# Kernel optimization log

Hardware: AMD Instinct MI355X
Metric: run time of the kernel (lower is better)

## Reference

```python
import jax, jax.numpy as jnp
import numpy as np

EPS = 1e-5


def hyper_graph_conv(x, elements, W, b):
    """x: [B, C, N] vertex features; elements: [M, 8] vertex ids per hex element.
    Gather 8 vertex features per element, apply Linear(8C -> 8Co) on the
    concatenated features, then scatter-mean the 8 outputs back to vertices.
    Returns [B, Co, N]."""
    B, C, N = x.shape
    M = elements.shape[0]
    Co = W.shape[0] // 8
    g = x[:, :, elements]                      # [B, C, M, 8]
    g = jnp.transpose(g, (0, 2, 3, 1)).reshape(B, M, 8 * C)   # [B, M, 8C]
    h = jnp.einsum('bmk,ok->bmo', g, W) + b    # [B, M, 8Co]
    h = h.reshape(B, M * 8, Co)                # per-(element,corner) vertex outputs
    flat = elements.reshape(-1)                # [M*8]
    out = jnp.zeros((B, N, Co), dtype=x.dtype).at[:, flat, :].add(h)
    cnt = jnp.zeros((N,), dtype=x.dtype).at[flat].add(1.0)
    out = out / jnp.maximum(cnt, 1.0)[None, :, None]
    return jnp.transpose(out, (0, 2, 1))       # [B, Co, N]


def batch_norm(x, gamma, beta):
    # BatchNorm1d in training mode over [B, C, N]: stats over (B, N)
    mean = jnp.mean(x, axis=(0, 2), keepdims=True)
    var = jnp.mean(jnp.square(x - mean), axis=(0, 2), keepdims=True)
    xn = (x - mean) * jax.lax.rsqrt(var + EPS)
    return xn * gamma[None, :, None] + beta[None, :, None]


def setup_inputs() -> dict:
    key = jax.random.key(0)
    ks = jax.random.split(key, 8)
    B, Cin, Cout, N, M = 4, 8, 16, 100000, 98304
    return {
        'x': jax.random.normal(ks[0], (B, Cin, N), dtype=jnp.float32),
        'elements': jax.random.randint(ks[1], (M, 8), 0, N, dtype=jnp.int32),
        'W1': jax.random.normal(ks[2], (8 * Cout, 8 * Cin), dtype=jnp.float32) * (1.0 / np.sqrt(8 * Cin)),
        'b1': jnp.zeros((8 * Cout,), dtype=jnp.float32),
        'gamma1': jnp.ones((Cout,), dtype=jnp.float32),
        'beta1': jnp.zeros((Cout,), dtype=jnp.float32),
        'W2': jax.random.normal(ks[3], (8 * Cout, 8 * Cout), dtype=jnp.float32) * (1.0 / np.sqrt(8 * Cout)),
        'b2': jnp.zeros((8 * Cout,), dtype=jnp.float32),
        'gamma2': jnp.ones((Cout,), dtype=jnp.float32),
        'beta2': jnp.zeros((Cout,), dtype=jnp.float32),
        'Wskip': jax.random.normal(ks[4], (Cout, Cin), dtype=jnp.float32) * (1.0 / np.sqrt(Cin)),
        'bskip': jnp.zeros((Cout,), dtype=jnp.float32),
    }


def reference(x, elements, W1, b1, gamma1, beta1, W2, b2, gamma2, beta2, Wskip, bskip):
    out = hyper_graph_conv(x, elements, W1, b1)        # [B, Cout, N]
    out = jax.nn.relu(batch_norm(out, gamma1, beta1))
    out = hyper_graph_conv(out, elements, W2, b2)      # [B, Cout, N]
    out = batch_norm(out, gamma2, beta2)
    skip = jnp.einsum('bcn,oc->bon', x, Wskip) + bskip[None, :, None]  # Conv1d k=1
    out = jax.nn.relu(out + skip)
    return out
```

## Files before the change

kernel.cpp:

```cpp
#include <hip/hip_runtime.h>

#define NB 4
#define CIN 8
#define CO 16
#define NV 100000
#define NM 98304
#define NPOS (NM*8)
#define NBLK ((NV+255)/256)
#define RED_NWV 8192

typedef short s16x8 __attribute__((ext_vector_type(8)));
typedef float f32x4 __attribute__((ext_vector_type(4)));
typedef unsigned short u16;
typedef unsigned int u32;

#define OFF_CNT   0
#define OFF_NEXT  400128
#define OFF_STAT  800256
#define OFF_ROWS  800640
#define OFF_BSUM  1200768
#define OFF_POS   1202432
#define OFF_XTB   4348160
#define OFF_W1B   10748160
#define OFF_W2B   10764544
#define OFF_H1    10797312
#define OFF_ACC   23597312
#define OFF_HBUF  49197312
#define WS_NEED   149860608

static __device__ __forceinline__ u16 f2bf(float f){
  union { float f; u32 u; } v; v.f = f;
  u32 r = v.u + 0x7fffu + ((v.u >> 16) & 1u);
  return (u16)(r >> 16);
}
static __device__ __forceinline__ float bf2f_lo(u32 w){
  union { u32 u; float f; } v; v.u = w << 16; return v.f;
}
static __device__ __forceinline__ float bf2f_hi(u32 w){
  union { u32 u; float f; } v; v.u = w & 0xffff0000u; return v.f;
}
static __device__ __forceinline__ u32 pk2(float a, float b){
  return (u32)f2bf(a) | (((u32)f2bf(b)) << 16);
}

__global__ __launch_bounds__(256) void k_hist(const int* __restrict__ elem,
    const float* __restrict__ W1, const float* __restrict__ W2,
    int* __restrict__ cnt, u16* __restrict__ w1b, u16* __restrict__ w2b)
{
  const int T1 = NPOS;
  const int T2 = T1 + 128*64;
  const int T3 = T2 + 128*128;
  int stride = gridDim.x*blockDim.x;
  for (int i = blockIdx.x*blockDim.x + threadIdx.x; i < T3; i += stride){
    if (i < T1) { atomicAdd(cnt + elem[i], 1); }
    else if (i < T2){ int j = i - T1; w1b[j] = f2bf(W1[j]); }
    else { int j = i - T2; w2b[j] = f2bf(W2[j]); }
  }
}

__global__ __launch_bounds__(256) void k_xt(const float* __restrict__ x, u16* __restrict__ xtb)
{
  __shared__ float tile[32][257];
  int t = threadIdx.x;
  int v0 = blockIdx.x*256;
  #pragma unroll
  for (int r = 0; r < 32; r++){
    int v = v0 + t;
    tile[r][t] = (v < NV) ? x[(size_t)r*NV + v] : 0.f;
  }
  __syncthreads();
  int v = v0 + t;
  if (v < NV){
    u16 o[32] __attribute__((aligned(16)));
    #pragma unroll
    for (int r = 0; r < 32; r++) o[r] = f2bf(tile[r][t]);
    uint4* dst = (uint4*)(xtb + (size_t)v*32);
    #pragma unroll
    for (int k = 0; k < 4; k++) dst[k] = *(uint4*)(o + k*8);
  }
}

__global__ __launch_bounds__(256) void k_scan_a(const int* __restrict__ cnt, int* __restrict__ bsum)
{
  int v = blockIdx.x*256 + threadIdx.x;
  int x = (v < NV) ? cnt[v] : 0;
  #pragma unroll
  for (int off = 32; off > 0; off >>= 1) x += __shfl_down(x, off);
  __shared__ int ls[4];
  int wid = threadIdx.x >> 6, lane = threadIdx.x & 63;
  if (lane == 0) ls[wid] = x;
  __syncthreads();
  if (threadIdx.x == 0) bsum[blockIdx.x] = ls[0] + ls[1] + ls[2] + ls[3];
}

__global__ void k_scan_b(int* __restrict__ bsum)
{
  int lane = threadIdx.x & 63;
  int base = 0;
  for (int i0 = 0; i0 < NBLK; i0 += 64){
    int i = i0 + lane;
    int xv = (i < NBLK) ? bsum[i] : 0;
    int incl = xv;
    #pragma unroll
    for (int off = 1; off <= 32; off <<= 1){
      int y = __shfl_up(incl, off);
      if (lane >= off) incl += y;
    }
    if (i < NBLK) bsum[i] = base + incl - xv;
    base += __shfl(incl, 63);
  }
}

__global__ __launch_bounds__(256) void k_scan_c(const int* __restrict__ cnt,
    const int* __restrict__ bsum, int* __restrict__ rows)
{
  int v = blockIdx.x*256 + threadIdx.x;
  int x = (v < NV) ? cnt[v] : 0;
  int incl = x;
  #pragma unroll
  for (int off = 1; off <= 32; off <<= 1){
    int y = __shfl_up(incl, off);
    if ((threadIdx.x & 63) >= off) incl += y;
  }
  __shared__ int wt[4];
  int wid = threadIdx.x >> 6, lane = threadIdx.x & 63;
  if (lane == 63) wt[wid] = incl;
  __syncthreads();
  int woff = 0;
  for (int w = 0; w < 4; w++) if (w < wid) woff += wt[w];
  if (v < NV) rows[v] = bsum[blockIdx.x] + woff + incl - x;
}

__global__ __launch_bounds__(256) void k_pos(const int* __restrict__ elem,
    const int* __restrict__ rows, int* __restrict__ next, int* __restrict__ pos)
{
  int i = blockIdx.x*256 + threadIdx.x;
  if (i < NPOS){
    int v = elem[i];
    int old = atomicAdd(next + v, 1);
    pos[i] = rows[v] + old;
  }
}

__global__ __launch_bounds__(256) void k_conv1(const int* __restrict__ elem,
    const u16* __restrict__ xtb, const u16* __restrict__ w1b,
    const float* __restrict__ b1, const int* __restrict__ pos, u16* __restrict__ hbuf)
{
  const int lane = threadIdx.x & 63;
  const int col = lane & 15, kg = lane >> 4, b = lane & 3;
  s16x8 wf[8][2];
  #pragma unroll
  for (int j2 = 0; j2 < 8; j2++)
    #pragma unroll
    for (int t = 0; t < 2; t++)
      wf[j2][t] = *(const s16x8*)(w1b + (j2*16 + col)*64 + t*32 + kg*8);
  float bb[8];
  #pragma unroll
  for (int j2 = 0; j2 < 8; j2++) bb[j2] = b1[j2*16 + col];

  int wave = (int)((blockIdx.x*blockDim.x + threadIdx.x) >> 6);
  int g0 = wave, g1 = wave + 12288;
  int ma0 = g0*4 + (col >> 2), ma1 = g1*4 + (col >> 2);
  int me0 = g0*4 + kg,         me1 = g1*4 + kg;

  int e00 = elem[ma0*8 + kg], e01 = elem[ma0*8 + 4 + kg];
  int e10 = elem[ma1*8 + kg], e11 = elem[ma1*8 + 4 + kg];
  int4 p0l = *(const int4*)(pos + me0*8), p0h = *(const int4*)(pos + me0*8 + 4);
  int4 p1l = *(const int4*)(pos + me1*8), p1h = *(const int4*)(pos + me1*8 + 4);
  s16x8 a00 = *(const s16x8*)(xtb + (size_t)e00*32 + b*8);
  s16x8 a01 = *(const s16x8*)(xtb + (size_t)e01*32 + b*8);
  s16x8 a10 = *(const s16x8*)(xtb + (size_t)e10*32 + b*8);
  s16x8 a11 = *(const s16x8*)(xtb + (size_t)e11*32 + b*8);

  int pe0[8] = {p0l.x,p0l.y,p0l.z,p0l.w,p0h.x,p0h.y,p0h.z,p0h.w};
  int pe1[8] = {p1l.x,p1l.y,p1l.z,p1l.w,p1h.x,p1h.y,p1h.z,p1h.w};

  #pragma unroll
  for (int j2 = 0; j2 < 8; j2++){
    f32x4 c = {0.f,0.f,0.f,0.f};
    c = __builtin_amdgcn_mfma_f32_16x16x32_bf16(a00, wf[j2][0], c, 0, 0, 0);
    c = __builtin_amdgcn_mfma_f32_16x16x32_bf16(a01, wf[j2][1], c, 0, 0, 0);
    uint2 d; d.x = pk2(c[0]+bb[j2], c[1]+bb[j2]); d.y = pk2(c[2]+bb[j2], c[3]+bb[j2]);
    *(uint2*)(hbuf + (size_t)pe0[j2]*64 + col*4) = d;
  }
  #pragma unroll
  for (int j2 = 0; j2 < 8; j2++){
    f32x4 c = {0.f,0.f,0.f,0.f};
    c = __builtin_amdgcn_mfma_f32_16x16x32_bf16(a10, wf[j2][0], c, 0, 0, 0);
    c = __builtin_amdgcn_mfma_f32_16x16x32_bf16(a11, wf[j2][1], c, 0, 0, 0);
    uint2 d; d.x = pk2(c[0]+bb[j2], c[1]+bb[j2]); d.y = pk2(c[2]+bb[j2], c[3]+bb[j2]);
    *(uint2*)(hbuf + (size_t)pe1[j2]*64 + col*4) = d;
  }
}

__global__ __launch_bounds__(256) void k_conv2(const int* __restrict__ elem,
    const u16* __restrict__ h1, const u16* __restrict__ w2b,
    const float* __restrict__ b2, const int* __restrict__ pos, u16* __restrict__ hbuf)
{
  __shared__ u16 wl[16384];
  #pragma unroll
  for (int r = 0; r < 8; r++){
    int q = threadIdx.x + 256*r;
    int j2t = q >> 6, ln = q & 63;
    int cc = ln & 15, kk = ln >> 4;
    int j2 = j2t >> 2, tt = j2t & 3;
    *(s16x8*)(wl + (size_t)q*8) =
        *(const s16x8*)(w2b + (j2*16 + cc)*128 + tt*32 + kk*8);
  }

  const int lane = threadIdx.x & 63;
  const int col = lane & 15, kg = lane >> 4, b = lane & 3;
  const int p = kg >> 1;
  const int c0 = (kg & 1)*8;
  float bb[8];
  #pragma unroll
  for (int j2 = 0; j2 < 8; j2++) bb[j2] = b2[j2*16 + col];

  int wave = (int)((blockIdx.x*blockDim.x + threadIdx.x) >> 6);
  int g0 = wave, g1 = wave + 12288;
  int ma0 = g0*4 + (col >> 2), ma1 = g1*4 + (col >> 2);
  int me0 = g0*4 + kg,         me1 = g1*4 + kg;

  int4 e0l = *(const int4*)(elem + ma0*8), e0h = *(const int4*)(elem + ma0*8 + 4);
  int4 e1l = *(const int4*)(elem + ma1*8), e1h = *(const int4*)(elem + ma1*8 + 4);
  int4 p0l = *(const int4*)(pos + me0*8),  p0h = *(const int4*)(pos + me0*8 + 4);
  int4 p1l = *(const int4*)(pos + me1*8),  p1h = *(const int4*)(pos + me1*8 + 4);

  int v00 = p ? e0l.y : e0l.x, v01 = p ? e0l.w : e0l.z;
  int v02 = p ? e0h.y : e0h.x, v03 = p ? e0h.w : e0h.z;
  int v10 = p ? e1l.y : e1l.x, v11 = p ? e1l.w : e1l.z;
  int v12 = p ? e1h.y : e1h.x, v13 = p ? e1h.w : e1h.z;

  s16x8 af0[4], af1[4];
  af0[0] = *(const s16x8*)(h1 + (size_t)v00*64 + b*16 + c0);
  af0[1] = *(const s16x8*)(h1 + (size_t)v01*64 + b*16 + c0);
  af0[2] = *(const s16x8*)(h1 + (size_t)v02*64 + b*16 + c0);
  af0[3] = *(const s16x8*)(h1 + (size_t)v03*64 + b*16 + c0);
  af1[0] = *(const s16x8*)(h1 + (size_t)v10*64 + b*16 + c0);
  af1[1] = *(const s16x8*)(h1 + (size_t)v11*64 + b*16 + c0);
  af1[2] = *(const s16x8*)(h1 + (size_t)v12*64 + b*16 + c0);
  af1[3] = *(const s16x8*)(h1 + (size_t)v13*64 + b*16 + c0);

  int pe0[8] = {p0l.x,p0l.y,p0l.z,p0l.w,p0h.x,p0h.y,p0h.z,p0h.w};
  int pe1[8] = {p1l.x,p1l.y,p1l.z,p1l.w,p1h.x,p1h.y,p1h.z,p1h.w};

  __syncthreads();

  #pragma unroll
  for (int j2 = 0; j2 < 8; j2++){
    s16x8 w0 = *(const s16x8*)(wl + ((size_t)(j2*4 + 0)*64 + lane)*8);
    s16x8 w1 = *(const s16x8*)(wl + ((size_t)(j2*4 + 1)*64 + lane)*8);
    s16x8 w2 = *(const s16x8*)(wl + ((size_t)(j2*4 + 2)*64 + lane)*8);
    s16x8 w3 = *(const s16x8*)(wl + ((size_t)(j2*4 + 3)*64 + lane)*8);
    f32x4 c = {0.f,0.f,0.f,0.f};
    c = __builtin_amdgcn_mfma_f32_16x16x32_bf16(af0[0], w0, c, 0, 0, 0);
    c = __builtin_amdgcn_mfma_f32_16x16x32_bf16(af0[1], w1, c, 0, 0, 0);
    c = __builtin_amdgcn_mfma_f32_16x16x32_bf16(af0[2], w2, c, 0, 0, 0);
    c = __builtin_amdgcn_mfma_f32_16x16x32_bf16(af0[3], w3, c, 0, 0, 0);
    uint2 d; d.x = pk2(c[0]+bb[j2], c[1]+bb[j2]); d.y = pk2(c[2]+bb[j2], c[3]+bb[j2]);
    *(uint2*)(hbuf + (size_t)pe0[j2]*64 + col*4) = d;
  }
  #pragma unroll
  for (int j2 = 0; j2 < 8; j2++){
    s16x8 w0 = *(const s16x8*)(wl + ((size_t)(j2*4 + 0)*64 + lane)*8);
    s16x8 w1 = *(const s16x8*)(wl + ((size_t)(j2*4 + 1)*64 + lane)*8);
    s16x8 w2 = *(const s16x8*)(wl + ((size_t)(j2*4 + 2)*64 + lane)*8);
    s16x8 w3 = *(const s16x8*)(wl + ((size_t)(j2*4 + 3)*64 + lane)*8);
    f32x4 c = {0.f,0.f,0.f,0.f};
    c = __builtin_amdgcn_mfma_f32_16x16x32_bf16(af1[0], w0, c, 0, 0, 0);
    c = __builtin_amdgcn_mfma_f32_16x16x32_bf16(af1[1], w1, c, 0, 0, 0);
    c = __builtin_amdgcn_mfma_f32_16x16x32_bf16(af1[2], w2, c, 0, 0, 0);
    c = __builtin_amdgcn_mfma_f32_16x16x32_bf16(af1[3], w3, c, 0, 0, 0);
    uint2 d; d.x = pk2(c[0]+bb[j2], c[1]+bb[j2]); d.y = pk2(c[2]+bb[j2], c[3]+bb[j2]);
    *(uint2*)(hbuf + (size_t)pe1[j2]*64 + col*4) = d;
  }
}

__global__ __launch_bounds__(256) void k_reduce(const u16* __restrict__ hbuf,
    const int* __restrict__ rows, float* __restrict__ acc, float* __restrict__ stat)
{
  int lane = threadIdx.x & 63, wid = threadIdx.x >> 6;
  int col = lane & 15, g = lane >> 4;
  int wv0 = (blockIdx.x*blockDim.x + threadIdx.x) >> 6;

  int vk = wv0 + lane*RED_NWV;
  int r0 = 0, r1 = 0;
  if (lane < 13 && vk < NV){
    r0 = rows[vk];
    r1 = (vk + 1 < NV) ? rows[vk + 1] : NPOS;
  }

  float st_s = 0.f, st_q = 0.f;
  __shared__ float ls[4][16], lq[4][16];

  #pragma unroll
  for (int k0 = 0; k0 < 16; k0 += 4){
    int rs[4], cc[4];
    #pragma unroll
    for (int j = 0; j < 4; j++){
      rs[j] = __shfl(r0, k0 + j);
      cc[j] = __shfl(r1, k0 + j) - rs[j];
    }
    int cmax = max(max(cc[0], cc[1]), max(cc[2], cc[3]));

    float A[4][4];
    #pragma unroll
    for (int j = 0; j < 4; j++){ A[j][0]=0.f; A[j][1]=0.f; A[j][2]=0.f; A[j][3]=0.f; }

    const u16* base[4];
    #pragma unroll
    for (int j = 0; j < 4; j++) base[j] = hbuf + (size_t)rs[j]*64 + col*4;

    for (int p = 0; p < cmax; p += 8){
      #pragma unroll
      for (int j = 0; j < 4; j++){
        int pa = p + g, pb = p + 4 + g;
        uint2 da = {0u,0u}, db = {0u,0u};
        if (pa < cc[j]) da = *(const uint2*)(base[j] + (size_t)pa*64);
        if (pb < cc[j]) db = *(const uint2*)(base[j] + (size_t)pb*64);
        A[j][0] += bf2f_lo(da.x) + bf2f_lo(db.x);
        A[j][1] += bf2f_hi(da.x) + bf2f_hi(db.x);
        A[j][2] += bf2f_lo(da.y) + bf2f_lo(db.y);
        A[j][3] += bf2f_hi(da.y) + bf2f_hi(db.y);
      }
    }

    #pragma unroll
    for (int j = 0; j < 4; j++){
      int v = wv0 + (k0 + j)*RED_NWV;
      if (v >= NV) continue;
      float s0 = A[j][0], s1 = A[j][1], s2 = A[j][2], s3 = A[j][3];
      s0 += __shfl_xor(s0,16); s0 += __shfl_xor(s0,32);
      s1 += __shfl_xor(s1,16); s1 += __shfl_xor(s1,32);
      s2 += __shfl_xor(s2,16); s2 += __shfl_xor(s2,32);
      s3 += __shfl_xor(s3,16); s3 += __shfl_xor(s3,32);
      float inv = 1.0f / fmaxf((float)cc[j], 1.0f);
      float val = (g==0 ? s0 : g==1 ? s1 : g==2 ? s2 : s3) * inv;
      acc[((size_t)g*NV + v)*16 + col] = val;
      st_s += val; st_q += val*val;
    }
  }

  st_s += __shfl_xor(st_s, 16); st_s += __shfl_xor(st_s, 32);
  st_q += __shfl_xor(st_q, 16); st_q += __shfl_xor(st_q, 32);
  if (lane < 16){ ls[wid][lane] = st_s; lq[wid][lane] = st_q; }
  __syncthreads();
  if (threadIdx.x < 32){
    int c2 = threadIdx.x & 15, which = threadIdx.x >> 4;
    float tot = 0.f;
    #pragma unroll
    for (int w = 0; w < 4; w++) tot += which ? lq[w][c2] : ls[w][c2];
    unsafeAtomicAdd(stat + which*16 + c2, tot);
  }
}

__global__ void k_finalize(float* __restrict__ stat, const float* __restrict__ gamma,
                           const float* __restrict__ beta)
{
  int co = threadIdx.x;
  if (co < 16){
    const float invn = 1.0f / (float)(NB*NV);
    float meanv = stat[co]*invn;
    float var   = stat[16+co]*invn - meanv*meanv;
    float sc = gamma[co]*rsqrtf(var + 1e-5f);
    stat[32+co] = sc;
    stat[48+co] = beta[co] - meanv*sc;
  }
}

__global__ __launch_bounds__(256) void k_apply1(const float* __restrict__ acc,
    const float* __restrict__ stat, u16* __restrict__ h1)
{
  int idx = blockIdx.x*256 + threadIdx.x;
  int v = idx >> 2, b = idx & 3;
  if (v >= NV) return;
  const f32x4* a4 = (const f32x4*)(acc + ((size_t)b*NV + v)*16);
  u16 o[16] __attribute__((aligned(16)));
  #pragma unroll
  for (int k = 0; k < 4; k++){
    f32x4 vv = a4[k];
    #pragma unroll
    for (int t = 0; t < 4; t++){
      int co = k*4 + t;
      float val = vv[t]*stat[32+co] + stat[48+co];
      o[co] = f2bf(fmaxf(val, 0.f));
    }
  }
  uint4* dst = (uint4*)(h1 + (size_t)v*64 + b*16);
  dst[0] = *(uint4*)(o);
  dst[1] = *(uint4*)(o + 8);
}

__global__ __launch_bounds__(256) void k_final(const float* __restrict__ acc,
    const float* __restrict__ stat, const float* __restrict__ x,
    const float* __restrict__ wsk, const float* __restrict__ bsk, float* __restrict__ out)
{
  int n = blockIdx.x*blockDim.x + threadIdx.x;
  int b = blockIdx.y;
  if (n >= NV) return;
  float xv[8];
  #pragma unroll
  for (int c = 0; c < 8; c++) xv[c] = x[((size_t)b*8 + c)*NV + n];
  const f32x4* a4 = (const f32x4*)(acc + ((size_t)b*NV + n)*16);
  #pragma unroll
  for (int k = 0; k < 4; k++){
    f32x4 v = a4[k];
    #pragma unroll
    for (int t = 0; t < 4; t++){
      int co = k*4 + t;
      float val = v[t]*stat[32+co] + stat[48+co] + bsk[co];
      #pragma unroll
      for (int c = 0; c < 8; c++) val += wsk[co*8+c]*xv[c];
      out[((size_t)b*16 + co)*NV + n] = fmaxf(val, 0.f);
    }
  }
}

extern "C" void kernel_launch(void* const* d_in, const int* in_sizes, int n_in,
                              void* d_out, int out_size, void* d_ws, size_t ws_size,
                              hipStream_t stream) {
  const float* x    = (const float*)d_in[0];
  const int*   elem = (const int*)  d_in[1];
  const float* W1   = (const float*)d_in[2];
  const float* b1   = (const float*)d_in[3];
  const float* g1   = (const float*)d_in[4];
  const float* be1  = (const float*)d_in[5];
  const float* W2   = (const float*)d_in[6];
  const float* b2   = (const float*)d_in[7];
  const float* g2   = (const float*)d_in[8];
  const float* be2  = (const float*)d_in[9];
  const float* Wsk  = (const float*)d_in[10];
  const float* bsk  = (const float*)d_in[11];
  float* out = (float*)d_out;

  if (ws_size < (size_t)WS_NEED) return;

  char* ws = (char*)d_ws;
  int*   cnt  = (int*)  (ws + OFF_CNT);
  int*   next = (int*)  (ws + OFF_NEXT);
  float* stat = (float*)(ws + OFF_STAT);
  int*   rows = (int*)  (ws + OFF_ROWS);
  int*   bsum = (int*)  (ws + OFF_BSUM);
  int*   pos  = (int*)  (ws + OFF_POS);
  u16*   xtb  = (u16*)  (ws + OFF_XTB);
  u16*   w1b  = (u16*)  (ws + OFF_W1B);
  u16*   w2b  = (u16*)  (ws + OFF_W2B);
  u16*   h1   = (u16*)  (ws + OFF_H1);
  float* acc  = (float*)(ws + OFF_ACC);
  u16*   hbuf = (u16*)  (ws + OFF_HBUF);

  hipMemsetAsync(ws, 0, OFF_STAT + 384, stream);

  k_hist<<<1024, 256, 0, stream>>>(elem, W1, W2, cnt, w1b, w2b);
  k_xt<<<NBLK, 256, 0, stream>>>(x, xtb);
  k_scan_a<<<NBLK, 256, 0, stream>>>(cnt, bsum);
  k_scan_b<<<1, 64, 0, stream>>>(bsum);
  k_scan_c<<<NBLK, 256, 0, stream>>>(cnt, bsum, rows);
  k_pos<<<NPOS/256, 256, 0, stream>>>(elem, rows, next, pos);

  k_conv1<<<3072, 256, 0, stream>>>(elem, xtb, w1b, b1, pos, hbuf);
  k_reduce<<<2048, 256, 0, stream>>>(hbuf, rows, acc, stat);
  k_finalize<<<1, 64, 0, stream>>>(stat, g1, be1);
  k_apply1<<<(NV*4 + 255)/256, 256, 0, stream>>>(acc, stat, h1);

  hipMemsetAsync(stat, 0, 128, stream);

  k_conv2<<<3072, 256, 0, stream>>>(elem, h1, w2b, b2, pos, hbuf);
  k_reduce<<<2048, 256, 0, stream>>>(hbuf, rows, acc, stat);
  k_finalize<<<1, 64, 0, stream>>>(stat, g2, be2);
  k_final<<<dim3((NV+255)/256, NB), 256, 0, stream>>>(acc, stat, x, Wsk, bsk, out);
}
```

Measured before the change: 275.3 us.

## Fuse prep kernels, drop scan and finalize launches, widen reduce loads

```diff
diff --git a/kernel.cpp b/kernel.cpp
--- a/kernel.cpp
+++ b/kernel.cpp
@@ -43,40 +43,39 @@
   return (u32)f2bf(a) | (((u32)f2bf(b)) << 16);
 }
 
-__global__ __launch_bounds__(256) void k_hist(const int* __restrict__ elem,
-    const float* __restrict__ W1, const float* __restrict__ W2,
-    int* __restrict__ cnt, u16* __restrict__ w1b, u16* __restrict__ w2b)
-{
-  const int T1 = NPOS;
-  const int T2 = T1 + 128*64;
-  const int T3 = T2 + 128*128;
-  int stride = gridDim.x*blockDim.x;
-  for (int i = blockIdx.x*blockDim.x + threadIdx.x; i < T3; i += stride){
-    if (i < T1) { atomicAdd(cnt + elem[i], 1); }
-    else if (i < T2){ int j = i - T1; w1b[j] = f2bf(W1[j]); }
-    else { int j = i - T2; w2b[j] = f2bf(W2[j]); }
-  }
-}
-
-__global__ __launch_bounds__(256) void k_xt(const float* __restrict__ x, u16* __restrict__ xtb)
+__global__ __launch_bounds__(256) void k_prep(const int* __restrict__ elem,
+    const float* __restrict__ x, const float* __restrict__ W1, const float* __restrict__ W2,
+    int* __restrict__ cnt, u16* __restrict__ xtb, u16* __restrict__ w1b, u16* __restrict__ w2b)
 {
   __shared__ float tile[32][257];
-  int t = threadIdx.x;
-  int v0 = blockIdx.x*256;
-  #pragma unroll
-  for (int r = 0; r < 32; r++){
+  if (blockIdx.x < NBLK){
+    int t = threadIdx.x;
+    int v0 = blockIdx.x*256;
+    #pragma unroll
+    for (int r = 0; r < 32; r++){
+      int v = v0 + t;
+      tile[r][t] = (v < NV) ? x[(size_t)r*NV + v] : 0.f;
+    }
+    __syncthreads();
     int v = v0 + t;
-    tile[r][t] = (v < NV) ? x[(size_t)r*NV + v] : 0.f;
-  }
-  __syncthreads();
-  int v = v0 + t;
-  if (v < NV){
-    u16 o[32] __attribute__((aligned(16)));
-    #pragma unroll
-    for (int r = 0; r < 32; r++) o[r] = f2bf(tile[r][t]);
-    uint4* dst = (uint4*)(xtb + (size_t)v*32);
-    #pragma unroll
-    for (int k = 0; k < 4; k++) dst[k] = *(uint4*)(o + k*8);
+    if (v < NV){
+      u16 o[32] __attribute__((aligned(16)));
+      #pragma unroll
+      for (int r = 0; r < 32; r++) o[r] = f2bf(tile[r][t]);
+      uint4* dst = (uint4*)(xtb + (size_t)v*32);
+      #pragma unroll
+      for (int k = 0; k < 4; k++) dst[k] = *(uint4*)(o + k*8);
+    }
+  } else {
+    const int T1 = NPOS;
+    const int T2 = T1 + 128*64;
+    const int T3 = T2 + 128*128;
+    int stride = (gridDim.x - NBLK)*256;
+    for (int i = (blockIdx.x - NBLK)*256 + threadIdx.x; i < T3; i += stride){
+      if (i < T1) { atomicAdd(cnt + elem[i], 1); }
+      else if (i < T2){ int j = i - T1; w1b[j] = f2bf(W1[j]); }
+      else { int j = i - T2; w2b[j] = f2bf(W2[j]); }
+    }
   }
 }
 
@@ -93,42 +92,32 @@
   if (threadIdx.x == 0) bsum[blockIdx.x] = ls[0] + ls[1] + ls[2] + ls[3];
 }
 
-__global__ void k_scan_b(int* __restrict__ bsum)
-{
-  int lane = threadIdx.x & 63;
-  int base = 0;
-  for (int i0 = 0; i0 < NBLK; i0 += 64){
-    int i = i0 + lane;
-    int xv = (i < NBLK) ? bsum[i] : 0;
-    int incl = xv;
-    #pragma unroll
-    for (int off = 1; off <= 32; off <<= 1){
-      int y = __shfl_up(incl, off);
-      if (lane >= off) incl += y;
-    }
-    if (i < NBLK) bsum[i] = base + incl - xv;
-    base += __shfl(incl, 63);
-  }
-}
-
 __global__ __launch_bounds__(256) void k_scan_c(const int* __restrict__ cnt,
     const int* __restrict__ bsum, int* __restrict__ rows)
 {
+  int wid = threadIdx.x >> 6, lane = threadIdx.x & 63;
   int v = blockIdx.x*256 + threadIdx.x;
   int x = (v < NV) ? cnt[v] : 0;
   int incl = x;
   #pragma unroll
   for (int off = 1; off <= 32; off <<= 1){
     int y = __shfl_up(incl, off);
-    if ((threadIdx.x & 63) >= off) incl += y;
+    if (lane >= off) incl += y;
   }
   __shared__ int wt[4];
-  int wid = threadIdx.x >> 6, lane = threadIdx.x & 63;
+  __shared__ int sbase;
   if (lane == 63) wt[wid] = incl;
+  if (threadIdx.x < 64){
+    int s = 0;
+    for (int i = threadIdx.x; i < blockIdx.x; i += 64) s += bsum[i];
+    #pragma unroll
+    for (int off = 32; off > 0; off >>= 1) s += __shfl_down(s, off);
+    if (threadIdx.x == 0) sbase = s;
+  }
   __syncthreads();
   int woff = 0;
   for (int w = 0; w < 4; w++) if (w < wid) woff += wt[w];
-  if (v < NV) rows[v] = bsum[blockIdx.x] + woff + incl - x;
+  if (v < NV) rows[v] = sbase + woff + incl - x;
 }
 
 __global__ __launch_bounds__(256) void k_pos(const int* __restrict__ elem,
@@ -280,7 +269,7 @@
     const int* __restrict__ rows, float* __restrict__ acc, float* __restrict__ stat)
 {
   int lane = threadIdx.x & 63, wid = threadIdx.x >> 6;
-  int col = lane & 15, g = lane >> 4;
+  int k8 = lane & 7, rg = lane >> 3;
   int wv0 = (blockIdx.x*blockDim.x + threadIdx.x) >> 6;
 
   int vk = wv0 + lane*RED_NWV;
@@ -290,60 +279,72 @@
     r1 = (vk + 1 < NV) ? rows[vk + 1] : NPOS;
   }
 
-  float st_s = 0.f, st_q = 0.f;
+  float st_s0 = 0.f, st_s1 = 0.f, st_q0 = 0.f, st_q1 = 0.f;
+
+  #pragma unroll
+  for (int k0 = 0; k0 < 16; k0 += 2){
+    int rsA = __shfl(r0, k0),     cA = __shfl(r1, k0)     - rsA;
+    int rsB = __shfl(r0, k0 + 1), cB = __shfl(r1, k0 + 1) - rsB;
+    int vA = wv0 + k0*RED_NWV, vB = wv0 + (k0 + 1)*RED_NWV;
+
+    float a0=0,a1=0,a2=0,a3=0,a4=0,a5=0,a6=0,a7=0;
+    float b0=0,b1=0,b2=0,b3=0,b4=0,b5=0,b6=0,b7=0;
+    const u16* pA = hbuf + (size_t)rsA*64 + lane*8;
+    const u16* pB = hbuf + (size_t)rsB*64 + lane*8;
+    int cm = max(cA, cB);
+    for (int p = 0; p < cm; p += 8){
+      uint4 dA = {0u,0u,0u,0u}, dB = {0u,0u,0u,0u};
+      if (p + rg < cA) dA = *(const uint4*)(pA + (size_t)p*64);
+      if (p + rg < cB) dB = *(const uint4*)(pB + (size_t)p*64);
+      a0 += bf2f_lo(dA.x); a1 += bf2f_hi(dA.x); a2 += bf2f_lo(dA.y); a3 += bf2f_hi(dA.y);
+      a4 += bf2f_lo(dA.z); a5 += bf2f_hi(dA.z); a6 += bf2f_lo(dA.w); a7 += bf2f_hi(dA.w);
+      b0 += bf2f_lo(dB.x); b1 += bf2f_hi(dB.x); b2 += bf2f_lo(dB.y); b3 += bf2f_hi(dB.y);
+      b4 += bf2f_lo(dB.z); b5 += bf2f_hi(dB.z); b6 += bf2f_lo(dB.w); b7 += bf2f_hi(dB.w);
+    }
+    #pragma unroll
+    for (int off = 8; off <= 32; off <<= 1){
+      a0 += __shfl_xor(a0, off); a1 += __shfl_xor(a1, off);
+      a2 += __shfl_xor(a2, off); a3 += __shfl_xor(a3, off);
+      a4 += __shfl_xor(a4, off); a5 += __shfl_xor(a5, off);
+      a6 += __shfl_xor(a6, off); a7 += __shfl_xor(a7, off);
+      b0 += __shfl_xor(b0, off); b1 += __shfl_xor(b1, off);
+      b2 += __shfl_xor(b2, off); b3 += __shfl_xor(b3, off);
+      b4 += __shfl_xor(b4, off); b5 += __shfl_xor(b5, off);
+      b6 += __shfl_xor(b6, off); b7 += __shfl_xor(b7, off);
+    }
+    if (lane < 8){
+      if (vA < NV){
+        float inv = 1.0f / fmaxf((float)cA, 1.0f);
+        float c0b[4] = {a0*inv, a1*inv, a2*inv, a3*inv};
+        float c1b[4] = {a4*inv, a5*inv, a6*inv, a7*inv};
+        #pragma unroll
+        for (int q = 0; q < 4; q++){
+          float2 w2; w2.x = c0b[q]; w2.y = c1b[q];
+          *(float2*)(acc + ((size_t)q*NV + vA)*16 + 2*k8) = w2;
+          st_s0 += c0b[q]; st_q0 += c0b[q]*c0b[q];
+          st_s1 += c1b[q]; st_q1 += c1b[q]*c1b[q];
+        }
+      }
+      if (vB < NV){
+        float inv = 1.0f / fmaxf((float)cB, 1.0f);
+        float c0b[4] = {b0*inv, b1*inv, b2*inv, b3*inv};
+        float c1b[4] = {b4*inv, b5*inv, b6*inv, b7*inv};
+        #pragma unroll
+        for (int q = 0; q < 4; q++){
+          float2 w2; w2.x = c0b[q]; w2.y = c1b[q];
+          *(float2*)(acc + ((size_t)q*NV + vB)*16 + 2*k8) = w2;
+          st_s0 += c0b[q]; st_q0 += c0b[q]*c0b[q];
+          st_s1 += c1b[q]; st_q1 += c1b[q]*c1b[q];
+        }
+      }
+    }
+  }
+
   __shared__ float ls[4][16], lq[4][16];
-
-  #pragma unroll
-  for (int k0 = 0; k0 < 16; k0 += 4){
-    int rs[4], cc[4];
-    #pragma unroll
-    for (int j = 0; j < 4; j++){
-      rs[j] = __shfl(r0, k0 + j);
-      cc[j] = __shfl(r1, k0 + j) - rs[j];
-    }
-    int cmax = max(max(cc[0], cc[1]), max(cc[2], cc[3]));
-
-    float A[4][4];
-    #pragma unroll
-    for (int j = 0; j < 4; j++){ A[j][0]=0.f; A[j][1]=0.f; A[j][2]=0.f; A[j][3]=0.f; }
-
-    const u16* base[4];
-    #pragma unroll
-    for (int j = 0; j < 4; j++) base[j] = hbuf + (size_t)rs[j]*64 + col*4;
-
-    for (int p = 0; p < cmax; p += 8){
-      #pragma unroll
-      for (int j = 0; j < 4; j++){
-        int pa = p + g, pb = p + 4 + g;
-        uint2 da = {0u,0u}, db = {0u,0u};
-        if (pa < cc[j]) da = *(const uint2*)(base[j] + (size_t)pa*64);
-        if (pb < cc[j]) db = *(const uint2*)(base[j] + (size_t)pb*64);
-        A[j][0] += bf2f_lo(da.x) + bf2f_lo(db.x);
-        A[j][1] += bf2f_hi(da.x) + bf2f_hi(db.x);
-        A[j][2] += bf2f_lo(da.y) + bf2f_lo(db.y);
-        A[j][3] += bf2f_hi(da.y) + bf2f_hi(db.y);
-      }
-    }
-
-    #pragma unroll
-    for (int j = 0; j < 4; j++){
-      int v = wv0 + (k0 + j)*RED_NWV;
-      if (v >= NV) continue;
-      float s0 = A[j][0], s1 = A[j][1], s2 = A[j][2], s3 = A[j][3];
-      s0 += __shfl_xor(s0,16); s0 += __shfl_xor(s0,32);
-      s1 += __shfl_xor(s1,16); s1 += __shfl_xor(s1,32);
-      s2 += __shfl_xor(s2,16); s2 += __shfl_xor(s2,32);
-      s3 += __shfl_xor(s3,16); s3 += __shfl_xor(s3,32);
-      float inv = 1.0f / fmaxf((float)cc[j], 1.0f);
-      float val = (g==0 ? s0 : g==1 ? s1 : g==2 ? s2 : s3) * inv;
-      acc[((size_t)g*NV + v)*16 + col] = val;
-      st_s += val; st_q += val*val;
-    }
-  }
-
-  st_s += __shfl_xor(st_s, 16); st_s += __shfl_xor(st_s, 32);
-  st_q += __shfl_xor(st_q, 16); st_q += __shfl_xor(st_q, 32);
-  if (lane < 16){ ls[wid][lane] = st_s; lq[wid][lane] = st_q; }
+  if (lane < 8){
+    ls[wid][2*k8] = st_s0; ls[wid][2*k8+1] = st_s1;
+    lq[wid][2*k8] = st_q0; lq[wid][2*k8+1] = st_q1;
+  }
   __syncthreads();
   if (threadIdx.x < 32){
     int c2 = threadIdx.x & 15, which = threadIdx.x >> 4;
@@ -354,23 +355,20 @@
   }
 }
 
-__global__ void k_finalize(float* __restrict__ stat, const float* __restrict__ gamma,
-                           const float* __restrict__ beta)
-{
-  int co = threadIdx.x;
-  if (co < 16){
+__global__ __launch_bounds__(256) void k_apply1(const float* __restrict__ acc,
+    const float* __restrict__ stat, const float* __restrict__ gamma,
+    const float* __restrict__ beta, u16* __restrict__ h1)
+{
+  __shared__ float sc[16], sh[16];
+  if (threadIdx.x < 16){
+    int co = threadIdx.x;
     const float invn = 1.0f / (float)(NB*NV);
-    float meanv = stat[co]*invn;
-    float var   = stat[16+co]*invn - meanv*meanv;
-    float sc = gamma[co]*rsqrtf(var + 1e-5f);
-    stat[32+co] = sc;
-    stat[48+co] = beta[co] - meanv*sc;
-  }
-}
-
-__global__ __launch_bounds__(256) void k_apply1(const float* __restrict__ acc,
-    const float* __restrict__ stat, u16* __restrict__ h1)
-{
+    float m = stat[co]*invn;
+    float var = stat[16+co]*invn - m*m;
+    float s = gamma[co]*rsqrtf(var + 1e-5f);
+    sc[co] = s; sh[co] = beta[co] - m*s;
+  }
+  __syncthreads();
   int idx = blockIdx.x*256 + threadIdx.x;
   int v = idx >> 2, b = idx & 3;
   if (v >= NV) return;
@@ -382,7 +380,7 @@
     #pragma unroll
     for (int t = 0; t < 4; t++){
       int co = k*4 + t;
-      float val = vv[t]*stat[32+co] + stat[48+co];
+      float val = vv[t]*sc[co] + sh[co];
       o[co] = f2bf(fmaxf(val, 0.f));
     }
   }
@@ -392,9 +390,20 @@
 }
 
 __global__ __launch_bounds__(256) void k_final(const float* __restrict__ acc,
-    const float* __restrict__ stat, const float* __restrict__ x,
+    const float* __restrict__ stat, const float* __restrict__ gamma,
+    const float* __restrict__ beta, const float* __restrict__ x,
     const float* __restrict__ wsk, const float* __restrict__ bsk, float* __restrict__ out)
 {
+  __shared__ float sc[16], sh[16];
+  if (threadIdx.x < 16){
+    int co = threadIdx.x;
+    const float invn = 1.0f / (float)(NB*NV);
+    float m = stat[co]*invn;
+    float var = stat[16+co]*invn - m*m;
+    float s = gamma[co]*rsqrtf(var + 1e-5f);
+    sc[co] = s; sh[co] = beta[co] - m*s + bsk[co];
+  }
+  __syncthreads();
   int n = blockIdx.x*blockDim.x + threadIdx.x;
   int b = blockIdx.y;
   if (n >= NV) return;
@@ -408,7 +417,7 @@
     #pragma unroll
     for (int t = 0; t < 4; t++){
       int co = k*4 + t;
-      float val = v[t]*stat[32+co] + stat[48+co] + bsk[co];
+      float val = v[t]*sc[co] + sh[co];
       #pragma unroll
       for (int c = 0; c < 8; c++) val += wsk[co*8+c]*xv[c];
       out[((size_t)b*16 + co)*NV + n] = fmaxf(val, 0.f);
@@ -451,22 +460,16 @@
 
   hipMemsetAsync(ws, 0, OFF_STAT + 384, stream);
 
-  k_hist<<<1024, 256, 0, stream>>>(elem, W1, W2, cnt, w1b, w2b);
-  k_xt<<<NBLK, 256, 0, stream>>>(x, xtb);
+  k_prep<<<NBLK + 1024, 256, 0, stream>>>(elem, x, W1, W2, cnt, xtb, w1b, w2b);
   k_scan_a<<<NBLK, 256, 0, stream>>>(cnt, bsum);
-  k_scan_b<<<1, 64, 0, stream>>>(bsum);
   k_scan_c<<<NBLK, 256, 0, stream>>>(cnt, bsum, rows);
   k_pos<<<NPOS/256, 256, 0, stream>>>(elem, rows, next, pos);
 
   k_conv1<<<3072, 256, 0, stream>>>(elem, xtb, w1b, b1, pos, hbuf);
   k_reduce<<<2048, 256, 0, stream>>>(hbuf, rows, acc, stat);
-  k_finalize<<<1, 64, 0, stream>>>(stat, g1, be1);
-  k_apply1<<<(NV*4 + 255)/256, 256, 0, stream>>>(acc, stat, h1);
-
-  hipMemsetAsync(stat, 0, 128, stream);
+  k_apply1<<<(NV*4 + 255)/256, 256, 0, stream>>>(acc, stat, g1, be1, h1);
 
   k_conv2<<<3072, 256, 0, stream>>>(elem, h1, w2b, b2, pos, hbuf);
-  k_reduce<<<2048, 256, 0, stream>>>(hbuf, rows, acc, stat);
-  k_finalize<<<1, 64, 0, stream>>>(stat, g2, be2);
-  k_final<<<dim3((NV+255)/256, NB), 256, 0, stream>>>(acc, stat, x, Wsk, bsk, out);
-}
+  k_reduce<<<2048, 256, 0, stream>>>(hbuf, rows, acc, stat + 32);
+  k_final<<<dim3((NV+255)/256, NB), 256, 0, stream>>>(acc, stat + 32, g2, be2, x, Wsk, bsk, out);
+}
```

Result: faster. 265.4 us (-3.6%).
